# Kernel tuning notes

Measured on AMD Instinct MI355X. Metric: run time of the kernel, lower is better.

Reference implementation:

```python
import jax, jax.numpy as jnp
import numpy as np

NEG_SLOPE = 0.01  # torch leaky_relu default
STEPS = 19

def _lrelu(x):
    return jnp.where(x >= 0, x, NEG_SLOPE * x)

def setup_inputs() -> dict:
    key = jax.random.key(0)
    ks = jax.random.split(key, 13)
    def lin(kw, kb, fan_in, fan_out):
        bound = 1.0 / np.sqrt(fan_in)
        W = jax.random.uniform(kw, (fan_in, fan_out), minval=-bound, maxval=bound, dtype=jnp.float32)
        b = jax.random.uniform(kb, (fan_out,), minval=-bound, maxval=bound, dtype=jnp.float32)
        return W, b
    Wh1, bh1 = lin(ks[0], ks[1], 2, 50)
    Wh2, bh2 = lin(ks[2], ks[3], 50, 20)
    Wh3, bh3 = lin(ks[4], ks[5], 20, 2)
    Wz1, bz1 = lin(ks[6], ks[7], 2, 50)
    Wz2, bz2 = lin(ks[8], ks[9], 50, 20)
    Wz3, bz3 = lin(ks[10], ks[11], 20, 2)
    w = jax.random.normal(ks[12], (1048576, 2), dtype=jnp.float32)
    return {"w": w,
            "Wh1": Wh1, "bh1": bh1, "Wh2": Wh2, "bh2": bh2, "Wh3": Wh3, "bh3": bh3,
            "Wz1": Wz1, "bz1": bz1, "Wz2": Wz2, "bz2": bz2, "Wz3": Wz3, "bz3": bz3}

def reference(w, Wh1, bh1, Wh2, bh2, Wh3, bh3, Wz1, bz1, Wz2, bz2, Wz3, bz3):
    def step(h, _):
        h = _lrelu(h @ Wh1 + bh1)          # [B,50]
        h = _lrelu(h @ Wh2 + bh2)          # [B,20]
        h = _lrelu(h @ Wh3 + bh3)          # [B,2]
        z = jax.nn.sigmoid(h @ Wz1 + bz1)  # [B,50]
        z = jax.nn.sigmoid(z @ Wz2 + bz2)  # [B,20]
        z = jax.nn.sigmoid(z @ Wz3 + bz3)  # [B,2]
        return h, z
    _, zs = jax.lax.scan(step, w, None, length=STEPS)  # zs: [19,B,2]
    return jnp.transpose(zs, (1, 0, 2))                # [B,19,2]
```

## Files before the change

kernel.cpp:

```cpp
#include <hip/hip_runtime.h>
#include <math.h>

#define STEPS 19
#define THREADS 256
#define L2E 1.44269504088896340736f

typedef _Float16 half8   __attribute__((ext_vector_type(8)));
typedef float    floatx4 __attribute__((ext_vector_type(4)));
typedef __fp16   half2_t __attribute__((ext_vector_type(2)));

#define WAVE_LDS 8192

#define WS_BH    0
#define WS_BZ    4096
#define WS_H1W0  8192
#define WS_H1W1  8292
#define WS_H1B   8392
#define WS_Z1W0  8492
#define WS_Z1W1  8592
#define WS_Z1B   8692
#define WS_WZ3   8792
#define WS_BZ3   8952

#define LDS_FENCE() asm volatile("" ::: "memory")

__device__ __forceinline__ float lrelu(float x) { return fmaxf(x, 0.01f * x); }
__device__ __forceinline__ float sigm2(float y) {
    return __builtin_amdgcn_rcpf(1.0f + __builtin_amdgcn_exp2f(y));
}
__device__ __forceinline__ unsigned int pkrtz_u(float a, float b) {
    return __builtin_bit_cast(unsigned int, __builtin_amdgcn_cvt_pkrtz(a, b));
}
__device__ __forceinline__ unsigned int packh2(float a, float b) {
    half2_t h; h.x = (__fp16)a; h.y = (__fp16)b;
    return __builtin_bit_cast(unsigned int, h);
}
__device__ __forceinline__ unsigned int h2bits(half2_t h) {
    return __builtin_bit_cast(unsigned int, h);
}
__device__ __forceinline__ half2_t bits2h(unsigned int u) {
    return __builtin_bit_cast(half2_t, u);
}

__device__ __forceinline__ half2_t sigm_h2(half2_t y) {
#if __has_builtin(__builtin_elementwise_exp2) && __has_builtin(__builtin_amdgcn_rcph)
    half2_t e = __builtin_elementwise_exp2(y);
    e = e + (half2_t){(__fp16)1.0f, (__fp16)1.0f};
    half2_t r;
    r.x = __builtin_amdgcn_rcph(e.x);
    r.y = __builtin_amdgcn_rcph(e.y);
    return r;
#else
    return bits2h(pkrtz_u(sigm2((float)y.x), sigm2((float)y.y)));
#endif
}

__global__ __launch_bounds__(256) void pack_kernel(
    const float* __restrict__ Wh1, const float* __restrict__ bh1,
    const float* __restrict__ Wh2, const float* __restrict__ bh2,
    const float* __restrict__ Wz1, const float* __restrict__ bz1,
    const float* __restrict__ Wz2, const float* __restrict__ bz2,
    const float* __restrict__ Wz3, const float* __restrict__ bz3,
    char* __restrict__ ws)
{
    const int t = threadIdx.x;
    for (int e = t; e < 512; e += 256) {
        const int layer = e >> 8, r = e & 255;
        const int u = r >> 7, kk = (r >> 6) & 1, lane = r & 63;
        const int n = u * 16 + (lane & 15);
        const float* W2 = layer ? Wz2 : Wh2;
        const float* b2 = layer ? bz2 : bh2;
        const float scale = layer ? -L2E : 1.0f;
        unsigned int dw[4];
        #pragma unroll
        for (int d = 0; d < 4; ++d) {
            float v[2];
            #pragma unroll
            for (int h = 0; h < 2; ++h) {
                const int k = kk * 32 + ((lane >> 4) & 3) * 8 + 2 * d + h;
                float x = 0.0f;
                if (n < 20) {
                    if (k < 50)       x = W2[k * 20 + n] * scale;
                    else if (k == 50) x = b2[n] * scale;
                }
                v[h] = x;
            }
            dw[d] = packh2(v[0], v[1]);
        }
        *(uint4*)(ws + (layer ? WS_BZ : WS_BH) + (size_t)((u * 2 + kk) * 64 + lane) * 16)
            = make_uint4(dw[0], dw[1], dw[2], dw[3]);
    }
    if (t < 25) {
        ((unsigned int*)(ws + WS_H1W0))[t] = packh2(Wh1[2 * t],      Wh1[2 * t + 1]);
        ((unsigned int*)(ws + WS_H1W1))[t] = packh2(Wh1[50 + 2 * t], Wh1[51 + 2 * t]);
        ((unsigned int*)(ws + WS_H1B))[t]  = packh2(bh1[2 * t],      bh1[2 * t + 1]);
        ((unsigned int*)(ws + WS_Z1W0))[t] = packh2(-L2E * Wz1[2 * t],      -L2E * Wz1[2 * t + 1]);
        ((unsigned int*)(ws + WS_Z1W1))[t] = packh2(-L2E * Wz1[50 + 2 * t], -L2E * Wz1[51 + 2 * t]);
        ((unsigned int*)(ws + WS_Z1B))[t]  = packh2(-L2E * bz1[2 * t],      -L2E * bz1[2 * t + 1]);
    }
    if (t < 40)  ((float*)(ws + WS_WZ3))[t] = -L2E * Wz3[t];
    if (t < 2)   ((float*)(ws + WS_BZ3))[t] = -L2E * bz3[t];
}

__global__ __launch_bounds__(THREADS)
__attribute__((amdgpu_waves_per_eu(2)))
void recurrent_kernel(
    const float* __restrict__ w,
    const float* __restrict__ Wh3, const float* __restrict__ bh3,
    const char* __restrict__ ws,
    float* __restrict__ out, int nrows)
{
    __shared__ __align__(16) char lds[4 * WAVE_LDS];
    const int t    = threadIdx.x;
    const int lane = t & 63;
    const int wid  = t >> 6;
    const int lq   = (lane >> 4) & 3;
    const int ll   = lane & 15;
    char* ldsw = lds + wid * WAVE_LDS;

    char* awb = ldsw + (lane >> 4) * 1024 + (lane & 15) * 16;
    const char* arb = ldsw + lane * 16;
    const int cmod = (ll < 4) ? (16 + ll) : (ll - 4);
    char* cw0 = ldsw + lq * 320 + ll * 4;
    char* cw1 = ldsw + lq * 320 + cmod * 4;
    const char* crb = ldsw + lane * 80;

    uint4 Bh[2][2], Bz[2][2];
    #pragma unroll
    for (int u = 0; u < 2; ++u)
        #pragma unroll
        for (int kk = 0; kk < 2; ++kk) {
            Bh[u][kk] = *(const uint4*)(ws + WS_BH + (size_t)((u * 2 + kk) * 64 + lane) * 16);
            Bz[u][kk] = *(const uint4*)(ws + WS_BZ + (size_t)((u * 2 + kk) * 64 + lane) * 16);
        }
    const unsigned int* W0p  = (const unsigned int*)(ws + WS_H1W0);
    const unsigned int* W1p  = (const unsigned int*)(ws + WS_H1W1);
    const unsigned int* B1p  = (const unsigned int*)(ws + WS_H1B);
    const unsigned int* ZW0p = (const unsigned int*)(ws + WS_Z1W0);
    const unsigned int* ZW1p = (const unsigned int*)(ws + WS_Z1W1);
    const unsigned int* ZB1p = (const unsigned int*)(ws + WS_Z1B);
    const float* Wz3s = (const float*)(ws + WS_WZ3);
    const float* bz3s = (const float*)(ws + WS_BZ3);

    const half2_t c001h = {(__fp16)0.01f, (__fp16)0.01f};
    const floatx4 ZC = {0.0f, 0.0f, 0.0f, 0.0f};

    const int row = blockIdx.x * THREADS + t;
    const bool ok = row < nrows;
    const float2 w2 = *(const float2*)(w + 2 * (size_t)(ok ? row : 0));
    float h0 = w2.x, h1 = w2.y;
    float* orow = out + (size_t)row * (STEPS * 2);

    #pragma unroll 1
    for (int s = 0; s < STEPS; ++s) {
        {
            const __fp16 h0h = (__fp16)h0, h1h = (__fp16)h1;
            const half2_t h00 = {h0h, h0h};
            const half2_t h11 = {h1h, h1h};
            #pragma unroll
            for (int c = 0; c < 6; ++c) {
                unsigned int dw[4];
                #pragma unroll
                for (int p = 0; p < 4; ++p) {
                    const int q = c * 4 + p;
                    half2_t v = h11 * bits2h(W1p[q]) + (h00 * bits2h(W0p[q]) + bits2h(B1p[q]));
                    v = __builtin_elementwise_max(v, v * c001h);
                    dw[p] = h2bits(v);
                }
                *(uint4*)(awb + (c >> 2) * 4096 + (c & 3) * 256)
                    = make_uint4(dw[0], dw[1], dw[2], dw[3]);
            }
            {
                half2_t v = h11 * bits2h(W1p[24]) + (h00 * bits2h(W0p[24]) + bits2h(B1p[24]));
                v = __builtin_elementwise_max(v, v * c001h);
                *(uint4*)(awb + 4096 + 2 * 256) = make_uint4(h2bits(v), 0x00003C00u, 0u, 0u);
            }
            *(uint4*)(awb + 4096 + 3 * 256) = make_uint4(0u, 0u, 0u, 0u);
        }
        LDS_FENCE();
        floatx4 C[4][2];
        #pragma unroll
        for (int mt = 0; mt < 4; ++mt) {
            const half8 A0 = __builtin_bit_cast(half8, *(const uint4*)(arb + mt * 1024));
            const half8 A1 = __builtin_bit_cast(half8, *(const uint4*)(arb + 4096 + mt * 1024));
            C[mt][0] = __builtin_amdgcn_mfma_f32_16x16x32_f16(A0, __builtin_bit_cast(half8, Bh[0][0]), ZC,       0, 0, 0);
            C[mt][0] = __builtin_amdgcn_mfma_f32_16x16x32_f16(A1, __builtin_bit_cast(half8, Bh[0][1]), C[mt][0], 0, 0, 0);
            C[mt][1] = __builtin_amdgcn_mfma_f32_16x16x32_f16(A0, __builtin_bit_cast(half8, Bh[1][0]), ZC,       0, 0, 0);
            C[mt][1] = __builtin_amdgcn_mfma_f32_16x16x32_f16(A1, __builtin_bit_cast(half8, Bh[1][1]), C[mt][1], 0, 0, 0);
        }
        LDS_FENCE();
        #pragma unroll
        for (int mt = 0; mt < 4; ++mt)
            #pragma unroll
            for (int i = 0; i < 4; ++i)
                *(float*)(cw1 + mt * 1280 + i * 80) = C[mt][1][i];
        LDS_FENCE();
        #pragma unroll
        for (int mt = 0; mt < 4; ++mt)
            #pragma unroll
            for (int i = 0; i < 4; ++i)
                *(float*)(cw0 + mt * 1280 + i * 80) = C[mt][0][i];
        LDS_FENCE();
        float a2[20];
        #pragma unroll
        for (int p = 0; p < 5; ++p) {
            const float4 v = *(const float4*)(crb + p * 16);
            a2[4 * p] = v.x; a2[4 * p + 1] = v.y; a2[4 * p + 2] = v.z; a2[4 * p + 3] = v.w;
        }
        LDS_FENCE();
        float nh0 = bh3[0], nh1 = bh3[1];
        #pragma unroll
        for (int i = 0; i < 20; ++i) {
            const float a = lrelu(a2[i]);
            nh0 = fmaf(a, Wh3[2 * i], nh0);
            nh1 = fmaf(a, Wh3[2 * i + 1], nh1);
        }
        h0 = lrelu(nh0); h1 = lrelu(nh1);

        {
            const __fp16 g0h = (__fp16)h0, g1h = (__fp16)h1;
            const half2_t g00 = {g0h, g0h};
            const half2_t g11 = {g1h, g1h};
            #pragma unroll
            for (int c = 0; c < 6; ++c) {
                unsigned int dw[4];
                #pragma unroll
                for (int p = 0; p < 4; ++p) {
                    const int q = c * 4 + p;
                    half2_t y = g11 * bits2h(ZW1p[q]) + (g00 * bits2h(ZW0p[q]) + bits2h(ZB1p[q]));
                    dw[p] = h2bits(sigm_h2(y));
                }
                *(uint4*)(awb + (c >> 2) * 4096 + (c & 3) * 256)
                    = make_uint4(dw[0], dw[1], dw[2], dw[3]);
            }
            {
                half2_t y = g11 * bits2h(ZW1p[24]) + (g00 * bits2h(ZW0p[24]) + bits2h(ZB1p[24]));
                *(uint4*)(awb + 4096 + 2 * 256)
                    = make_uint4(h2bits(sigm_h2(y)), 0x00003C00u, 0u, 0u);
            }
            *(uint4*)(awb + 4096 + 3 * 256) = make_uint4(0u, 0u, 0u, 0u);
        }
        LDS_FENCE();
        #pragma unroll
        for (int mt = 0; mt < 4; ++mt) {
            const half8 A0 = __builtin_bit_cast(half8, *(const uint4*)(arb + mt * 1024));
            const half8 A1 = __builtin_bit_cast(half8, *(const uint4*)(arb + 4096 + mt * 1024));
            C[mt][0] = __builtin_amdgcn_mfma_f32_16x16x32_f16(A0, __builtin_bit_cast(half8, Bz[0][0]), ZC,       0, 0, 0);
            C[mt][0] = __builtin_amdgcn_mfma_f32_16x16x32_f16(A1, __builtin_bit_cast(half8, Bz[0][1]), C[mt][0], 0, 0, 0);
            C[mt][1] = __builtin_amdgcn_mfma_f32_16x16x32_f16(A0, __builtin_bit_cast(half8, Bz[1][0]), ZC,       0, 0, 0);
            C[mt][1] = __builtin_amdgcn_mfma_f32_16x16x32_f16(A1, __builtin_bit_cast(half8, Bz[1][1]), C[mt][1], 0, 0, 0);
        }
        LDS_FENCE();
        #pragma unroll
        for (int mt = 0; mt < 4; ++mt)
            #pragma unroll
            for (int i = 0; i < 4; ++i)
                *(float*)(cw1 + mt * 1280 + i * 80) = C[mt][1][i];
        LDS_FENCE();
        #pragma unroll
        for (int mt = 0; mt < 4; ++mt)
            #pragma unroll
            for (int i = 0; i < 4; ++i)
                *(float*)(cw0 + mt * 1280 + i * 80) = C[mt][0][i];
        LDS_FENCE();
        #pragma unroll
        for (int p = 0; p < 5; ++p) {
            const float4 v = *(const float4*)(crb + p * 16);
            a2[4 * p] = v.x; a2[4 * p + 1] = v.y; a2[4 * p + 2] = v.z; a2[4 * p + 3] = v.w;
        }
        LDS_FENCE();
        float zo0 = bz3s[0], zo1 = bz3s[1];
        #pragma unroll
        for (int i = 0; i < 20; ++i) {
            const float zz = sigm2(a2[i]);
            zo0 = fmaf(zz, Wz3s[2 * i], zo0);
            zo1 = fmaf(zz, Wz3s[2 * i + 1], zo1);
        }
        if (ok) {
            float2 o; o.x = sigm2(zo0); o.y = sigm2(zo1);
            *(float2*)(orow + 2 * s) = o;
        }
    }
}

extern "C" void kernel_launch(void* const* d_in, const int* in_sizes, int n_in,
                              void* d_out, int out_size, void* d_ws, size_t ws_size,
                              hipStream_t stream) {
    const float* w   = (const float*)d_in[0];
    const float* Wh1 = (const float*)d_in[1];
    const float* bh1 = (const float*)d_in[2];
    const float* Wh2 = (const float*)d_in[3];
    const float* bh2 = (const float*)d_in[4];
    const float* Wh3 = (const float*)d_in[5];
    const float* bh3 = (const float*)d_in[6];
    const float* Wz1 = (const float*)d_in[7];
    const float* bz1 = (const float*)d_in[8];
    const float* Wz2 = (const float*)d_in[9];
    const float* bz2 = (const float*)d_in[10];
    const float* Wz3 = (const float*)d_in[11];
    const float* bz3 = (const float*)d_in[12];
    float* out = (float*)d_out;

    pack_kernel<<<1, 256, 0, stream>>>(Wh1, bh1, Wh2, bh2, Wz1, bz1, Wz2, bz2,
                                       Wz3, bz3, (char*)d_ws);

    const int nrows = in_sizes[0] / 2;
    const int blocks = (nrows + THREADS - 1) / THREADS;
    recurrent_kernel<<<blocks, THREADS, 0, stream>>>(
        w, Wh3, bh3, (const char*)d_ws, out, nrows);
}
```

Measured before the change: 628.8 us.

## Split layer-2 K into two passes to shrink per-wave LDS and raise occupancy

Layer-1 activations were staged in one 8 KB per-wave LDS buffer holding both K-halves at once. They are now written and consumed in two passes that reuse a single 4 KB region, with the second half's MFMAs accumulating into the first half's results. Per-wave LDS drops to 5120 bytes and the waves-per-EU hint rises from 2 to 8, so more blocks can be resident and hide latency. In exchange each layer pays extra LDS round trips and a serial dependency between the halves, and the tighter register budget from the higher occupancy hint may cause spills.

```diff
diff --git a/kernel.cpp b/kernel.cpp
--- a/kernel.cpp
+++ b/kernel.cpp
@@ -9,7 +9,7 @@
 typedef float    floatx4 __attribute__((ext_vector_type(4)));
 typedef __fp16   half2_t __attribute__((ext_vector_type(2)));
 
-#define WAVE_LDS 8192
+#define WAVE_LDS 5120
 
 #define WS_BH    0
 #define WS_BZ    4096
@@ -103,7 +103,7 @@
 }
 
 __global__ __launch_bounds__(THREADS)
-__attribute__((amdgpu_waves_per_eu(2)))
+__attribute__((amdgpu_waves_per_eu(8)))
 void recurrent_kernel(
     const float* __restrict__ w,
     const float* __restrict__ Wh3, const float* __restrict__ bh3,
@@ -153,12 +153,14 @@
 
     #pragma unroll 1
     for (int s = 0; s < STEPS; ++s) {
+        floatx4 C[4][2];
+
         {
             const __fp16 h0h = (__fp16)h0, h1h = (__fp16)h1;
             const half2_t h00 = {h0h, h0h};
             const half2_t h11 = {h1h, h1h};
             #pragma unroll
-            for (int c = 0; c < 6; ++c) {
+            for (int c = 0; c < 4; ++c) {
                 unsigned int dw[4];
                 #pragma unroll
                 for (int p = 0; p < 4; ++p) {
@@ -167,26 +169,41 @@
                     v = __builtin_elementwise_max(v, v * c001h);
                     dw[p] = h2bits(v);
                 }
-                *(uint4*)(awb + (c >> 2) * 4096 + (c & 3) * 256)
-                    = make_uint4(dw[0], dw[1], dw[2], dw[3]);
+                *(uint4*)(awb + c * 256) = make_uint4(dw[0], dw[1], dw[2], dw[3]);
+            }
+            LDS_FENCE();
+            #pragma unroll
+            for (int mt = 0; mt < 4; ++mt) {
+                const half8 A0 = __builtin_bit_cast(half8, *(const uint4*)(arb + mt * 1024));
+                C[mt][0] = __builtin_amdgcn_mfma_f32_16x16x32_f16(A0, __builtin_bit_cast(half8, Bh[0][0]), ZC, 0, 0, 0);
+                C[mt][1] = __builtin_amdgcn_mfma_f32_16x16x32_f16(A0, __builtin_bit_cast(half8, Bh[1][0]), ZC, 0, 0, 0);
+            }
+            LDS_FENCE();
+            #pragma unroll
+            for (int c = 4; c < 6; ++c) {
+                unsigned int dw[4];
+                #pragma unroll
+                for (int p = 0; p < 4; ++p) {
+                    const int q = c * 4 + p;
+                    half2_t v = h11 * bits2h(W1p[q]) + (h00 * bits2h(W0p[q]) + bits2h(B1p[q]));
+                    v = __builtin_elementwise_max(v, v * c001h);
+                    dw[p] = h2bits(v);
+                }
+                *(uint4*)(awb + (c - 4) * 256) = make_uint4(dw[0], dw[1], dw[2], dw[3]);
             }
             {
                 half2_t v = h11 * bits2h(W1p[24]) + (h00 * bits2h(W0p[24]) + bits2h(B1p[24]));
                 v = __builtin_elementwise_max(v, v * c001h);
-                *(uint4*)(awb + 4096 + 2 * 256) = make_uint4(h2bits(v), 0x00003C00u, 0u, 0u);
-            }
-            *(uint4*)(awb + 4096 + 3 * 256) = make_uint4(0u, 0u, 0u, 0u);
-        }
-        LDS_FENCE();
-        floatx4 C[4][2];
-        #pragma unroll
-        for (int mt = 0; mt < 4; ++mt) {
-            const half8 A0 = __builtin_bit_cast(half8, *(const uint4*)(arb + mt * 1024));
-            const half8 A1 = __builtin_bit_cast(half8, *(const uint4*)(arb + 4096 + mt * 1024));
-            C[mt][0] = __builtin_amdgcn_mfma_f32_16x16x32_f16(A0, __builtin_bit_cast(half8, Bh[0][0]), ZC,       0, 0, 0);
-            C[mt][0] = __builtin_amdgcn_mfma_f32_16x16x32_f16(A1, __builtin_bit_cast(half8, Bh[0][1]), C[mt][0], 0, 0, 0);
-            C[mt][1] = __builtin_amdgcn_mfma_f32_16x16x32_f16(A0, __builtin_bit_cast(half8, Bh[1][0]), ZC,       0, 0, 0);
-            C[mt][1] = __builtin_amdgcn_mfma_f32_16x16x32_f16(A1, __builtin_bit_cast(half8, Bh[1][1]), C[mt][1], 0, 0, 0);
+                *(uint4*)(awb + 2 * 256) = make_uint4(h2bits(v), 0x00003C00u, 0u, 0u);
+            }
+            *(uint4*)(awb + 3 * 256) = make_uint4(0u, 0u, 0u, 0u);
+            LDS_FENCE();
+            #pragma unroll
+            for (int mt = 0; mt < 4; ++mt) {
+                const half8 A1 = __builtin_bit_cast(half8, *(const uint4*)(arb + mt * 1024));
+                C[mt][0] = __builtin_amdgcn_mfma_f32_16x16x32_f16(A1, __builtin_bit_cast(half8, Bh[0][1]), C[mt][0], 0, 0, 0);
+                C[mt][1] = __builtin_amdgcn_mfma_f32_16x16x32_f16(A1, __builtin_bit_cast(half8, Bh[1][1]), C[mt][1], 0, 0, 0);
+            }
         }
         LDS_FENCE();
         #pragma unroll
@@ -222,7 +239,7 @@
             const half2_t g00 = {g0h, g0h};
             const half2_t g11 = {g1h, g1h};
             #pragma unroll
-            for (int c = 0; c < 6; ++c) {
+            for (int c = 0; c < 4; ++c) {
                 unsigned int dw[4];
                 #pragma unroll
                 for (int p = 0; p < 4; ++p) {
@@ -230,25 +247,39 @@
                     half2_t y = g11 * bits2h(ZW1p[q]) + (g00 * bits2h(ZW0p[q]) + bits2h(ZB1p[q]));
                     dw[p] = h2bits(sigm_h2(y));
                 }
-                *(uint4*)(awb + (c >> 2) * 4096 + (c & 3) * 256)
-                    = make_uint4(dw[0], dw[1], dw[2], dw[3]);
+                *(uint4*)(awb + c * 256) = make_uint4(dw[0], dw[1], dw[2], dw[3]);
+            }
+            LDS_FENCE();
+            #pragma unroll
+            for (int mt = 0; mt < 4; ++mt) {
+                const half8 A0 = __builtin_bit_cast(half8, *(const uint4*)(arb + mt * 1024));
+                C[mt][0] = __builtin_amdgcn_mfma_f32_16x16x32_f16(A0, __builtin_bit_cast(half8, Bz[0][0]), ZC, 0, 0, 0);
+                C[mt][1] = __builtin_amdgcn_mfma_f32_16x16x32_f16(A0, __builtin_bit_cast(half8, Bz[1][0]), ZC, 0, 0, 0);
+            }
+            LDS_FENCE();
+            #pragma unroll
+            for (int c = 4; c < 6; ++c) {
+                unsigned int dw[4];
+                #pragma unroll
+                for (int p = 0; p < 4; ++p) {
+                    const int q = c * 4 + p;
+                    half2_t y = g11 * bits2h(ZW1p[q]) + (g00 * bits2h(ZW0p[q]) + bits2h(ZB1p[q]));
+                    dw[p] = h2bits(sigm_h2(y));
+                }
+                *(uint4*)(awb + (c - 4) * 256) = make_uint4(dw[0], dw[1], dw[2], dw[3]);
             }
             {
                 half2_t y = g11 * bits2h(ZW1p[24]) + (g00 * bits2h(ZW0p[24]) + bits2h(ZB1p[24]));
-                *(uint4*)(awb + 4096 + 2 * 256)
-                    = make_uint4(h2bits(sigm_h2(y)), 0x00003C00u, 0u, 0u);
-            }
-            *(uint4*)(awb + 4096 + 3 * 256) = make_uint4(0u, 0u, 0u, 0u);
-        }
-        LDS_FENCE();
-        #pragma unroll
-        for (int mt = 0; mt < 4; ++mt) {
-            const half8 A0 = __builtin_bit_cast(half8, *(const uint4*)(arb + mt * 1024));
-            const half8 A1 = __builtin_bit_cast(half8, *(const uint4*)(arb + 4096 + mt * 1024));
-            C[mt][0] = __builtin_amdgcn_mfma_f32_16x16x32_f16(A0, __builtin_bit_cast(half8, Bz[0][0]), ZC,       0, 0, 0);
-            C[mt][0] = __builtin_amdgcn_mfma_f32_16x16x32_f16(A1, __builtin_bit_cast(half8, Bz[0][1]), C[mt][0], 0, 0, 0);
-            C[mt][1] = __builtin_amdgcn_mfma_f32_16x16x32_f16(A0, __builtin_bit_cast(half8, Bz[1][0]), ZC,       0, 0, 0);
-            C[mt][1] = __builtin_amdgcn_mfma_f32_16x16x32_f16(A1, __builtin_bit_cast(half8, Bz[1][1]), C[mt][1], 0, 0, 0);
+                *(uint4*)(awb + 2 * 256) = make_uint4(h2bits(sigm_h2(y)), 0x00003C00u, 0u, 0u);
+            }
+            *(uint4*)(awb + 3 * 256) = make_uint4(0u, 0u, 0u, 0u);
+            LDS_FENCE();
+            #pragma unroll
+            for (int mt = 0; mt < 4; ++mt) {
+                const half8 A1 = __builtin_bit_cast(half8, *(const uint4*)(arb + mt * 1024));
+                C[mt][0] = __builtin_amdgcn_mfma_f32_16x16x32_f16(A1, __builtin_bit_cast(half8, Bz[0][1]), C[mt][0], 0, 0, 0);
+                C[mt][1] = __builtin_amdgcn_mfma_f32_16x16x32_f16(A1, __builtin_bit_cast(half8, Bz[1][1]), C[mt][1], 0, 0, 0);
+            }
         }
         LDS_FENCE();
         #pragma unroll
```

Result: slower. 1.061 ms (+68.8%).
